# Performance work log

Measured on AMD Instinct MI355X. Metric: run time of the kernel, lower is better.

Reference implementation:

```python
import jax, jax.numpy as jnp
import numpy as np

B, N, M = 256, 2207, 16          # graphs per batch, nodes per graph, mid_channel
E = 16777216                      # total edges in the batched graph
C1, C2 = 12, 4                    # global_conv1_dim, global_conv2_dim
H1, H2 = 256, 64                  # FC hidden sizes
EPS = 1e-5                        # LayerNorm / BatchNorm eps
BN_SCALE = 1.0 / np.sqrt(1.0 + EPS)  # eval BatchNorm with running_mean=0, running_var=1


def setup_inputs() -> dict:
    ks = jax.random.split(jax.random.key(0), 16)
    def nrm(i, shape, s):
        return jax.random.normal(ks[i], shape, jnp.float32) * s
    return {
        "x": jax.random.normal(ks[0], (B * N, 1), jnp.float32),
        "edge_index": jax.random.randint(ks[1], (2, E), 0, B * N, dtype=jnp.int32),
        "edge_weight": jax.random.uniform(ks[2], (E,), jnp.float32),
        # GraphConv: lin_rel (with bias) on aggregated neighbors + lin_root on self
        "w_root": nrm(3, (1, M), 0.5),
        "w_rel": nrm(4, (1, M), 0.5),
        "b_rel": jnp.full((M,), 0.01, jnp.float32),
        # LayerNorm over (num_nodes, mid_channel)
        "ln_g": jnp.ones((N, M), jnp.float32),
        "ln_b": jnp.zeros((N, M), jnp.float32),
        # 1x1 conv stacks
        "gc1_w": nrm(5, (C1, M), 0.3), "gc1_b": nrm(6, (C1,), 0.1),
        "bn1_g": jnp.ones((C1,), jnp.float32), "bn1_b": jnp.zeros((C1,), jnp.float32),
        "gc2_w": nrm(7, (C2, C1), 0.3), "gc2_b": nrm(8, (C2,), 0.1),
        "bn2_g": jnp.ones((C2,), jnp.float32), "bn2_b": jnp.zeros((C2,), jnp.float32),
        # FC stack (weights stored [in, out])
        "fc_w1": nrm(9, (C2 * N, H1), 0.02), "fc_b1": jnp.full((H1,), 0.01, jnp.float32),
        "fbn1_g": jnp.ones((H1,), jnp.float32), "fbn1_b": jnp.zeros((H1,), jnp.float32),
        "fc_w2": nrm(10, (H1, H2), 0.1), "fc_b2": jnp.full((H2,), 0.01, jnp.float32),
        "fbn2_g": jnp.ones((H2,), jnp.float32), "fbn2_b": jnp.zeros((H2,), jnp.float32),
        "fc1_w": nrm(11, (H2, 1), 0.1), "fc1_b": jnp.full((1,), 0.01, jnp.float32),
    }


def reference(x, edge_index, edge_weight, w_root, w_rel, b_rel, ln_g, ln_b,
              gc1_w, gc1_b, bn1_g, bn1_b, gc2_w, gc2_b, bn2_g, bn2_b,
              fc_w1, fc_b1, fbn1_g, fbn1_b, fc_w2, fc_b2, fbn2_g, fbn2_b,
              fc1_w, fc1_b):
    src, dst = edge_index[0], edge_index[1]
    # GraphConv: gather source features, weight, scatter-add to destinations
    agg = jax.ops.segment_sum(x[src] * edge_weight[:, None], dst, num_segments=B * N)
    h = jax.nn.relu(agg @ w_rel + b_rel + x @ w_root)          # [B*N, M]
    h = h.reshape(B, N, M)
    # LayerNorm over (N, M) per sample (biased variance, as in torch)
    mu = h.mean(axis=(1, 2), keepdims=True)
    var = ((h - mu) ** 2).mean(axis=(1, 2), keepdims=True)
    h = (h - mu) * jax.lax.rsqrt(var + EPS) * ln_g + ln_b
    h = h.transpose(0, 2, 1)                                   # [B, M, N]
    # 1x1 conv -> relu -> eval-BN (rm=0, rv=1)
    y = jax.nn.relu(jnp.einsum('oc,bcn->bon', gc1_w, h) + gc1_b[None, :, None])
    y = y * (BN_SCALE * bn1_g)[None, :, None] + bn1_b[None, :, None]
    y = jax.nn.relu(jnp.einsum('oc,bcn->bon', gc2_w, y) + gc2_b[None, :, None])
    y = y * (BN_SCALE * bn2_g)[None, :, None] + bn2_b[None, :, None]
    z = y.reshape(B, C2 * N)                                   # channel-major flatten, matches torch view
    z = z @ fc_w1 + fc_b1
    z = jax.nn.relu(z * (BN_SCALE * fbn1_g) + fbn1_b)
    z = z @ fc_w2 + fc_b2
    z = jax.nn.relu(z * (BN_SCALE * fbn2_g) + fbn2_b)
    return z @ fc1_w + fc1_b                                   # [B, 1]
```

## Files before the change

### kernel.cpp

```cpp
#include <hip/hip_runtime.h>
#include <hip/hip_bf16.h>

#define BB   256
#define NN   2207
#define MM   16
#define EE   16777216
#define CC1  12
#define CC2  4
#define HH1  256
#define HH2  64
#define KK1  (CC2*NN)
#define LN_EPS 1e-5f
#define BN_SCALE 0.9999950000374997f
#define NBK  256
#define MAGIC 1946067ull
#define EPB  4096
#define TPB  512
#define EPT  (EPB/TPB)
#define NBLK (EE/EPB)

static __device__ __forceinline__ unsigned bucket_of(int d) {
    return (unsigned)(((unsigned long long)(unsigned)d * MAGIC) >> 32);
}

__global__ __launch_bounds__(TPB, 8)
void k_place2(const int* __restrict__ src, const int* __restrict__ dst,
              const float* __restrict__ ew, const float* __restrict__ x,
              uint2* __restrict__ recs, unsigned short* __restrict__ stab)
{
    __shared__ __align__(16) uint2 pl[EPB];
    __shared__ unsigned int hist[NBK], start[NBK];
    __shared__ unsigned int wtot[4];

    const int t = threadIdx.x;
    if (t < NBK) hist[t] = 0;
    __syncthreads();

    const int i4base = blockIdx.x * (EPB/4);
    unsigned pk[EPT];
    float    pv[EPT];
    #pragma unroll
    for (int q = 0; q < EPT/4; ++q) {
        int i4 = i4base + q*TPB + t;
        int4   s4 = reinterpret_cast<const int4*>(src)[i4];
        int4   d4 = reinterpret_cast<const int4*>(dst)[i4];
        float4 w4 = reinterpret_cast<const float4*>(ew)[i4];
        {
            unsigned b_ = bucket_of(d4.x);
            unsigned r_ = atomicAdd(&hist[b_], 1u);
            pk[q*4+0] = (b_ << 24) | (r_ << 12) | (unsigned)(d4.x - (int)(b_*NN));
            pv[q*4+0] = x[s4.x] * w4.x;
        }
        {
            unsigned b_ = bucket_of(d4.y);
            unsigned r_ = atomicAdd(&hist[b_], 1u);
            pk[q*4+1] = (b_ << 24) | (r_ << 12) | (unsigned)(d4.y - (int)(b_*NN));
            pv[q*4+1] = x[s4.y] * w4.y;
        }
        {
            unsigned b_ = bucket_of(d4.z);
            unsigned r_ = atomicAdd(&hist[b_], 1u);
            pk[q*4+2] = (b_ << 24) | (r_ << 12) | (unsigned)(d4.z - (int)(b_*NN));
            pv[q*4+2] = x[s4.z] * w4.z;
        }
        {
            unsigned b_ = bucket_of(d4.w);
            unsigned r_ = atomicAdd(&hist[b_], 1u);
            pk[q*4+3] = (b_ << 24) | (r_ << 12) | (unsigned)(d4.w - (int)(b_*NN));
            pv[q*4+3] = x[s4.w] * w4.w;
        }
    }
    __syncthreads();

    if (t < NBK) {
        unsigned h = hist[t], v = h;
        #pragma unroll
        for (int off = 1; off < 64; off <<= 1) {
            unsigned u = __shfl_up(v, off);
            if ((t & 63) >= off) v += u;
        }
        start[t] = v - h;
        if ((t & 63) == 63) wtot[t >> 6] = v;
    }
    __syncthreads();
    if (t < NBK) {
        const int w = t >> 6;
        unsigned wo = 0;
        if (w > 0) wo += wtot[0];
        if (w > 1) wo += wtot[1];
        if (w > 2) wo += wtot[2];
        start[t] += wo;
        stab[blockIdx.x * NBK + t] = (unsigned short)(start[t]);
    }
    __syncthreads();

    #pragma unroll
    for (int e = 0; e < EPT; ++e) {
        unsigned b_ = pk[e] >> 24;
        unsigned r_ = (pk[e] >> 12) & 0xFFFu;
        pl[start[b_] + r_] = make_uint2(pk[e] & 0xFFFu, __float_as_uint(pv[e]));
    }
    __syncthreads();

    uint4* dst4 = reinterpret_cast<uint4*>(recs + (size_t)blockIdx.x * EPB);
    const uint4* src4 = reinterpret_cast<const uint4*>(pl);
    #pragma unroll
    for (int q = 0; q < EPB/2/TPB; ++q)
        dst4[q*TPB + t] = src4[q*TPB + t];
}

#define RTPB 256
__global__ __launch_bounds__(RTPB, 8)
void k_replay2(const uint2* __restrict__ recs, const unsigned short* __restrict__ stab,
               float* __restrict__ paggr, int rspl)
{
    __shared__ float acc[NN];
    const int t = threadIdx.x;
    const int j = blockIdx.x & (NBK - 1);
    const int r = blockIdx.x >> 8;
    const int kpr = NBLK / rspl;
    for (int n = t; n < NN; n += RTPB) acc[n] = 0.f;
    __syncthreads();

    const int gid = t >> 4, l16 = t & 15;
    const int kb0 = r * kpr;
    for (int kb_i = gid; kb_i < kpr; kb_i += RTPB/16) {
        const int kb = kb0 + kb_i;
        unsigned s0 = stab[(size_t)kb * NBK + j];
        unsigned s1 = (j < NBK-1) ? (unsigned)stab[(size_t)kb * NBK + j + 1]
                                  : (unsigned)EPB;
        const uint2* rp = recs + (size_t)kb * EPB;
        for (unsigned u = s0 + (unsigned)l16; u < s1; u += 16u) {
            uint2 rec = rp[u];
            atomicAdd(&acc[rec.x], __uint_as_float(rec.y));
        }
    }
    __syncthreads();
    float* pa = paggr + ((size_t)r * NBK + j) * NN;
    for (int n = t; n < NN; n += RTPB) pa[n] = acc[n];
}

__global__ __launch_bounds__(512)
void k_ln_conv(const float* __restrict__ x, const float* __restrict__ paggr,
              const float* __restrict__ w_root, const float* __restrict__ w_rel,
              const float* __restrict__ b_rel,
              const float* __restrict__ ln_g, const float* __restrict__ ln_b,
              const float* __restrict__ gc1_w, const float* __restrict__ gc1_b,
              const float* __restrict__ bn1_g, const float* __restrict__ bn1_b,
              const float* __restrict__ gc2_w, const float* __restrict__ gc2_b,
              const float* __restrict__ bn2_g, const float* __restrict__ bn2_b,
              float* __restrict__ z, int rspl)
{
    __shared__ float xs[NN], acc[NN];
    __shared__ float gw1[CC1*MM], gb1[CC1], sb1[CC1], tb1[CC1];
    __shared__ float gw2[CC2*CC1], gb2[CC2], sb2[CC2], tb2[CC2];
    __shared__ float redS[8], redQ[8];
    __shared__ float s_mu, s_rs;

    const int b = blockIdx.x, t = threadIdx.x;
    const float* xb = x + b*NN;
    for (int n = t; n < NN; n += 512) {
        xs[n] = xb[n];
        float a = 0.f;
        for (int r = 0; r < rspl; ++r)
            a += paggr[((size_t)r * NBK + b) * NN + n];
        acc[n] = a;
    }
    if (t < CC1*MM) gw1[t] = gc1_w[t];
    if (t >= 192 && t < 192+CC1) { int o = t-192; gb1[o]=gc1_b[o]; sb1[o]=BN_SCALE*bn1_g[o]; tb1[o]=bn1_b[o]; }
    if (t >= 208 && t < 208+CC2*CC1) gw2[t-208] = gc2_w[t-208];
    if (t >= 240 && t < 240+CC2) { int p=t-240; gb2[p]=gc2_b[p]; sb2[p]=BN_SCALE*bn2_g[p]; tb2[p]=bn2_b[p]; }

    float wr[MM], br[MM], wo[MM];
    #pragma unroll
    for (int m = 0; m < MM; ++m) { wr[m]=w_rel[m]; br[m]=b_rel[m]; wo[m]=w_root[m]; }
    __syncthreads();

    float S = 0.f, Q = 0.f;
    for (int n = t; n < NN; n += 512) {
        float a = acc[n], xv = xs[n];
        #pragma unroll
        for (int m = 0; m < MM; ++m) {
            float h = fmaxf(fmaf(a, wr[m], fmaf(xv, wo[m], br[m])), 0.f);
            S += h; Q += h*h;
        }
    }
    #pragma unroll
    for (int off = 32; off; off >>= 1) { S += __shfl_down(S, off); Q += __shfl_down(Q, off); }
    if ((t & 63) == 0) { redS[t>>6] = S; redQ[t>>6] = Q; }
    __syncthreads();
    if (t == 0) {
        float SS = 0.f, QQ = 0.f;
        #pragma unroll
        for (int i = 0; i < 8; ++i) { SS += redS[i]; QQ += redQ[i]; }
        const float inv = 1.f / (float)(NN*MM);
        float mu = SS * inv;
        float var = QQ * inv - mu*mu;
        s_mu = mu; s_rs = rsqrtf(var + LN_EPS);
    }
    __syncthreads();
    const float mu = s_mu, rs = s_rs;

    float* zb = z + (size_t)b * KK1;
    for (int n = t; n < NN; n += 512) {
        float a = acc[n], xv = xs[n];
        float hn[MM];
        const float4* g4  = reinterpret_cast<const float4*>(ln_g + n*MM);
        const float4* be4 = reinterpret_cast<const float4*>(ln_b + n*MM);
        #pragma unroll
        for (int q = 0; q < 4; ++q) {
            float4 g = g4[q], be = be4[q];
            float gg[4]  = {g.x, g.y, g.z, g.w};
            float bb_[4] = {be.x, be.y, be.z, be.w};
            #pragma unroll
            for (int j = 0; j < 4; ++j) {
                int m = q*4 + j;
                float h = fmaxf(fmaf(a, wr[m], fmaf(xv, wo[m], br[m])), 0.f);
                hn[m] = (h - mu) * rs * gg[j] + bb_[j];
            }
        }
        float y1[CC1];
        #pragma unroll
        for (int o = 0; o < CC1; ++o) {
            float a1 = gb1[o];
            #pragma unroll
            for (int m = 0; m < MM; ++m) a1 = fmaf(gw1[o*MM+m], hn[m], a1);
            y1[o] = fmaxf(a1, 0.f) * sb1[o] + tb1[o];
        }
        #pragma unroll
        for (int p = 0; p < CC2; ++p) {
            float a2 = gb2[p];
            #pragma unroll
            for (int o = 0; o < CC1; ++o) a2 = fmaf(gw2[p*CC1+o], y1[o], a2);
            zb[p*NN + n] = fmaxf(a2, 0.f) * sb2[p] + tb2[p];
        }
    }
}

#define GK_CHUNK 288
__global__ __launch_bounds__(256)
void k_fc1_part(const float* __restrict__ z, const float* __restrict__ W1,
                float* __restrict__ out1_part)
{
    __shared__ float zs[64*36];
    __shared__ float ws_[32*68];
    const int bt = blockIdx.x, jt = blockIdx.y, ks = blockIdx.z;
    const int t = threadIdx.x;
    const int tb = t >> 4, tj = t & 15;
    const int k0 = ks * GK_CHUNK;
    const int kend = min(k0 + GK_CHUNK, KK1);
    float acc[4][4] = {};
    const int zrow = t >> 2, zcol = (t & 3) * 8;
    const int wrow = t >> 3, wcol = (t & 7) * 8;

    for (int kc = k0; kc < kend; kc += 32) {
        const float* zsrc = z + (size_t)(bt*64 + zrow)*KK1 + kc + zcol;
        #pragma unroll
        for (int q = 0; q < 2; ++q) {
            int k = kc + zcol + q*4;
            float4 v;
            if (k + 3 < kend) v = *reinterpret_cast<const float4*>(zsrc + q*4);
            else {
                v.x = (k+0 < kend) ? zsrc[q*4+0] : 0.f;
                v.y = (k+1 < kend) ? zsrc[q*4+1] : 0.f;
                v.z = (k+2 < kend) ? zsrc[q*4+2] : 0.f;
                v.w = (k+3 < kend) ? zsrc[q*4+3] : 0.f;
            }
            *reinterpret_cast<float4*>(&zs[zrow*36 + zcol + q*4]) = v;
        }
        {
            int k = kc + wrow;
            const float* wsrc = W1 + (size_t)k*HH1 + jt*64 + wcol;
            #pragma unroll
            for (int q = 0; q < 2; ++q) {
                float4 v;
                if (k < kend) v = *reinterpret_cast<const float4*>(wsrc + q*4);
                else v = float4{0.f,0.f,0.f,0.f};
                *reinterpret_cast<float4*>(&ws_[wrow*68 + wcol + q*4]) = v;
            }
        }
        __syncthreads();
        #pragma unroll
        for (int kk = 0; kk < 32; ++kk) {
            float4 w4 = *reinterpret_cast<const float4*>(&ws_[kk*68 + tj*4]);
            float zv[4], wv[4] = {w4.x, w4.y, w4.z, w4.w};
            #pragma unroll
            for (int ib = 0; ib < 4; ++ib) zv[ib] = zs[(tb*4+ib)*36 + kk];
            #pragma unroll
            for (int ib = 0; ib < 4; ++ib)
                #pragma unroll
                for (int ij = 0; ij < 4; ++ij)
                    acc[ib][ij] = fmaf(zv[ib], wv[ij], acc[ib][ij]);
        }
        __syncthreads();
    }
    #pragma unroll
    for (int ib = 0; ib < 4; ++ib) {
        int row = bt*64 + tb*4 + ib;
        float4 v = make_float4(acc[ib][0], acc[ib][1], acc[ib][2], acc[ib][3]);
        *reinterpret_cast<float4*>(
            &out1_part[((size_t)ks*256 + row)*HH1 + jt*64 + tj*4]) = v;
    }
}

__global__ __launch_bounds__(256)
void k_tail_part(const float* __restrict__ out1_part,
            const float* __restrict__ fc_b1, const float* __restrict__ fbn1_g,
            const float* __restrict__ fbn1_b,
            const float* __restrict__ W2, const float* __restrict__ fc_b2,
            const float* __restrict__ fbn2_g, const float* __restrict__ fbn2_b,
            const float* __restrict__ fc1_w, const float* __restrict__ fc1_b,
            float* __restrict__ out)
{
    __shared__ float o1s[HH1];
    const int b = blockIdx.x, t = threadIdx.x;
    float raw = fc_b1[t];
    #pragma unroll 4
    for (int ks = 0; ks < 31; ++ks)
        raw += out1_part[((size_t)ks*256 + b)*HH1 + t];
    o1s[t] = fmaxf(raw * (BN_SCALE * fbn1_g[t]) + fbn1_b[t], 0.f);
    __syncthreads();
    if (t < HH2) {
        float acc = fc_b2[t];
        #pragma unroll 4
        for (int j = 0; j < HH1; ++j) acc = fmaf(o1s[j], W2[j*HH2 + t], acc);
        float v2 = fmaxf(acc * (BN_SCALE * fbn2_g[t]) + fbn2_b[t], 0.f);
        float c = v2 * fc1_w[t];
        #pragma unroll
        for (int off = 32; off; off >>= 1) c += __shfl_down(c, off);
        if (t == 0) out[b] = c + fc1_b[0];
    }
}

__global__ __launch_bounds__(256)
void k_edge(const int* __restrict__ src, const int* __restrict__ dst,
            const float* __restrict__ ew, const float* __restrict__ x,
            float* __restrict__ agg)
{
    int i = blockIdx.x * 256 + threadIdx.x;
    const int4   s4 = reinterpret_cast<const int4*>(src)[i];
    const int4   d4 = reinterpret_cast<const int4*>(dst)[i];
    const float4 w4 = reinterpret_cast<const float4*>(ew)[i];
    unsafeAtomicAdd(&agg[d4.x], x[s4.x] * w4.x);
    unsafeAtomicAdd(&agg[d4.y], x[s4.y] * w4.y);
    unsafeAtomicAdd(&agg[d4.z], x[s4.z] * w4.z);
    unsafeAtomicAdd(&agg[d4.w], x[s4.w] * w4.w);
}

__global__ __launch_bounds__(256)
void k_sample(const float* __restrict__ x, const float* __restrict__ agg,
              const float* __restrict__ w_root, const float* __restrict__ w_rel,
              const float* __restrict__ b_rel,
              const float* __restrict__ ln_g, const float* __restrict__ ln_b,
              const float* __restrict__ gc1_w, const float* __restrict__ gc1_b,
              const float* __restrict__ bn1_g, const float* __restrict__ bn1_b,
              const float* __restrict__ gc2_w, const float* __restrict__ gc2_b,
              const float* __restrict__ bn2_g, const float* __restrict__ bn2_b,
              float* __restrict__ z)
{
    __shared__ float xs[NN], as[NN];
    __shared__ float gw1[CC1*MM], gb1[CC1], sb1[CC1], tb1[CC1];
    __shared__ float gw2[CC2*CC1], gb2[CC2], sb2[CC2], tb2[CC2];
    __shared__ float redS[4], redQ[4];
    __shared__ float s_mu, s_rs;

    const int b = blockIdx.x, t = threadIdx.x;
    const float* xb = x + b*NN;
    const float* ab = agg + b*NN;
    for (int n = t; n < NN; n += 256) { xs[n] = xb[n]; as[n] = ab[n]; }
    if (t < CC1*MM) gw1[t] = gc1_w[t];
    if (t >= 192 && t < 192+CC1) { int o = t-192; gb1[o]=gc1_b[o]; sb1[o]=BN_SCALE*bn1_g[o]; tb1[o]=bn1_b[o]; }
    if (t >= 208 && t < 208+CC2*CC1) gw2[t-208] = gc2_w[t-208];
    if (t >= 240 && t < 240+CC2) { int p=t-240; gb2[p]=gc2_b[p]; sb2[p]=BN_SCALE*bn2_g[p]; tb2[p]=bn2_b[p]; }

    float wr[MM], br[MM], wo[MM];
    #pragma unroll
    for (int m = 0; m < MM; ++m) { wr[m]=w_rel[m]; br[m]=b_rel[m]; wo[m]=w_root[m]; }
    __syncthreads();

    float S = 0.f, Q = 0.f;
    for (int n = t; n < NN; n += 256) {
        float a = as[n], xv = xs[n];
        #pragma unroll
        for (int m = 0; m < MM; ++m) {
            float h = fmaxf(fmaf(a, wr[m], fmaf(xv, wo[m], br[m])), 0.f);
            S += h; Q += h*h;
        }
    }
    #pragma unroll
    for (int off = 32; off; off >>= 1) { S += __shfl_down(S, off); Q += __shfl_down(Q, off); }
    if ((t & 63) == 0) { redS[t>>6] = S; redQ[t>>6] = Q; }
    __syncthreads();
    if (t == 0) {
        float SS = redS[0]+redS[1]+redS[2]+redS[3];
        float QQ = redQ[0]+redQ[1]+redQ[2]+redQ[3];
        const float inv = 1.f / (float)(NN*MM);
        float mu = SS * inv;
        float var = QQ * inv - mu*mu;
        s_mu = mu; s_rs = rsqrtf(var + LN_EPS);
    }
    __syncthreads();
    const float mu = s_mu, rs = s_rs;

    float* zb = z + (size_t)b * KK1;
    for (int n = t; n < NN; n += 256) {
        float a = as[n], xv = xs[n];
        float hn[MM];
        const float4* g4  = reinterpret_cast<const float4*>(ln_g + n*MM);
        const float4* be4 = reinterpret_cast<const float4*>(ln_b + n*MM);
        #pragma unroll
        for (int q = 0; q < 4; ++q) {
            float4 g = g4[q], be = be4[q];
            float gg[4]  = {g.x, g.y, g.z, g.w};
            float bb_[4] = {be.x, be.y, be.z, be.w};
            #pragma unroll
            for (int j = 0; j < 4; ++j) {
                int m = q*4 + j;
                float h = fmaxf(fmaf(a, wr[m], fmaf(xv, wo[m], br[m])), 0.f);
                hn[m] = (h - mu) * rs * gg[j] + bb_[j];
            }
        }
        float y1[CC1];
        #pragma unroll
        for (int o = 0; o < CC1; ++o) {
            float a1 = gb1[o];
            #pragma unroll
            for (int m = 0; m < MM; ++m) a1 = fmaf(gw1[o*MM+m], hn[m], a1);
            y1[o] = fmaxf(a1, 0.f) * sb1[o] + tb1[o];
        }
        #pragma unroll
        for (int p = 0; p < CC2; ++p) {
            float a2 = gb2[p];
            #pragma unroll
            for (int o = 0; o < CC1; ++o) a2 = fmaf(gw2[p*CC1+o], y1[o], a2);
            zb[p*NN + n] = fmaxf(a2, 0.f) * sb2[p] + tb2[p];
        }
    }
}

__global__ __launch_bounds__(256)
void k_fc1(const float* __restrict__ z, const float* __restrict__ W1,
           float* __restrict__ out1_raw)
{
    __shared__ float zs[64*36];
    __shared__ float ws_[32*68];
    const int bt = blockIdx.x, jt = blockIdx.y, ks = blockIdx.z;
    const int t = threadIdx.x;
    const int tb = t >> 4, tj = t & 15;
    const int k0 = ks * GK_CHUNK;
    const int kend = min(k0 + GK_CHUNK, KK1);
    float acc[4][4] = {};
    const int zrow = t >> 2, zcol = (t & 3) * 8;
    const int wrow = t >> 3, wcol = (t & 7) * 8;

    for (int kc = k0; kc < kend; kc += 32) {
        const float* zsrc = z + (size_t)(bt*64 + zrow)*KK1 + kc + zcol;
        #pragma unroll
        for (int q = 0; q < 2; ++q) {
            int k = kc + zcol + q*4;
            float4 v;
            if (k + 3 < kend) v = *reinterpret_cast<const float4*>(zsrc + q*4);
            else {
                v.x = (k+0 < kend) ? zsrc[q*4+0] : 0.f;
                v.y = (k+1 < kend) ? zsrc[q*4+1] : 0.f;
                v.z = (k+2 < kend) ? zsrc[q*4+2] : 0.f;
                v.w = (k+3 < kend) ? zsrc[q*4+3] : 0.f;
            }
            *reinterpret_cast<float4*>(&zs[zrow*36 + zcol + q*4]) = v;
        }
        {
            int k = kc + wrow;
            const float* wsrc = W1 + (size_t)k*HH1 + jt*64 + wcol;
            #pragma unroll
            for (int q = 0; q < 2; ++q) {
                float4 v;
                if (k < kend) v = *reinterpret_cast<const float4*>(wsrc + q*4);
                else v = float4{0.f,0.f,0.f,0.f};
                *reinterpret_cast<float4*>(&ws_[wrow*68 + wcol + q*4]) = v;
            }
        }
        __syncthreads();
        #pragma unroll
        for (int kk = 0; kk < 32; ++kk) {
            float4 w4 = *reinterpret_cast<const float4*>(&ws_[kk*68 + tj*4]);
            float zv[4], wv[4] = {w4.x, w4.y, w4.z, w4.w};
            #pragma unroll
            for (int ib = 0; ib < 4; ++ib) zv[ib] = zs[(tb*4+ib)*36 + kk];
            #pragma unroll
            for (int ib = 0; ib < 4; ++ib)
                #pragma unroll
                for (int ij = 0; ij < 4; ++ij)
                    acc[ib][ij] = fmaf(zv[ib], wv[ij], acc[ib][ij]);
        }
        __syncthreads();
    }
    #pragma unroll
    for (int ib = 0; ib < 4; ++ib) {
        int row = bt*64 + tb*4 + ib;
        #pragma unroll
        for (int ij = 0; ij < 4; ++ij)
            unsafeAtomicAdd(&out1_raw[row*HH1 + jt*64 + tj*4 + ij], acc[ib][ij]);
    }
}

__global__ __launch_bounds__(256)
void k_tail(const float* __restrict__ out1_raw,
            const float* __restrict__ fc_b1, const float* __restrict__ fbn1_g,
            const float* __restrict__ fbn1_b,
            const float* __restrict__ W2, const float* __restrict__ fc_b2,
            const float* __restrict__ fbn2_g, const float* __restrict__ fbn2_b,
            const float* __restrict__ fc1_w, const float* __restrict__ fc1_b,
            float* __restrict__ out)
{
    __shared__ float o1s[HH1];
    const int b = blockIdx.x, t = threadIdx.x;
    float raw = out1_raw[b*HH1 + t] + fc_b1[t];
    o1s[t] = fmaxf(raw * (BN_SCALE * fbn1_g[t]) + fbn1_b[t], 0.f);
    __syncthreads();
    if (t < HH2) {
        float acc = fc_b2[t];
        #pragma unroll 4
        for (int j = 0; j < HH1; ++j) acc = fmaf(o1s[j], W2[j*HH2 + t], acc);
        float v2 = fmaxf(acc * (BN_SCALE * fbn2_g[t]) + fbn2_b[t], 0.f);
        float c = v2 * fc1_w[t];
        #pragma unroll
        for (int off = 32; off; off >>= 1) c += __shfl_down(c, off);
        if (t == 0) out[b] = c + fc1_b[0];
    }
}

extern "C" void kernel_launch(void* const* d_in, const int* in_sizes, int n_in,
                              void* d_out, int out_size, void* d_ws, size_t ws_size,
                              hipStream_t stream)
{
    const float* x      = (const float*)d_in[0];
    const int*   ei     = (const int*)  d_in[1];
    const float* ew     = (const float*)d_in[2];
    const float* w_root = (const float*)d_in[3];
    const float* w_rel  = (const float*)d_in[4];
    const float* b_rel  = (const float*)d_in[5];
    const float* ln_g   = (const float*)d_in[6];
    const float* ln_b   = (const float*)d_in[7];
    const float* gc1_w  = (const float*)d_in[8];
    const float* gc1_b  = (const float*)d_in[9];
    const float* bn1_g  = (const float*)d_in[10];
    const float* bn1_b  = (const float*)d_in[11];
    const float* gc2_w  = (const float*)d_in[12];
    const float* gc2_b  = (const float*)d_in[13];
    const float* bn2_g  = (const float*)d_in[14];
    const float* bn2_b  = (const float*)d_in[15];
    const float* fc_w1  = (const float*)d_in[16];
    const float* fc_b1  = (const float*)d_in[17];
    const float* fbn1_g = (const float*)d_in[18];
    const float* fbn1_b = (const float*)d_in[19];
    const float* fc_w2  = (const float*)d_in[20];
    const float* fc_b2  = (const float*)d_in[21];
    const float* fbn2_g = (const float*)d_in[22];
    const float* fbn2_b = (const float*)d_in[23];
    const float* fc1_w  = (const float*)d_in[24];
    const float* fc1_b  = (const float*)d_in[25];
    float* out = (float*)d_out;

    char* ws = (char*)d_ws;
    const size_t off_recs  = 0;
    const size_t off_stab  = off_recs + (size_t)NBLK*EPB*8;
    const size_t off_paggr = off_stab + (size_t)NBLK*NBK*2;
    const size_t o1p_sz    = (size_t)31*HH1*256*4;

    int rspl = 8;
    size_t pg_sz   = (size_t)rspl*NBK*NN*4;
    if (pg_sz < o1p_sz) pg_sz = o1p_sz;
    size_t off_zbuf = off_paggr + pg_sz;
    size_t need     = off_zbuf + (size_t)BB*KK1*4;
    if (ws_size < need) {
        rspl = 4;
        pg_sz = (size_t)rspl*NBK*NN*4;
        off_zbuf = off_paggr + pg_sz;
        need = off_zbuf + (size_t)BB*KK1*4;
    }

    if (ws_size >= need) {
        uint2*          recs  = (uint2*)(ws + off_recs);
        unsigned short* stab  = (unsigned short*)(ws + off_stab);
        float*          paggr = (float*)(ws + off_paggr);
        float*          zbuf  = (float*)(ws + off_zbuf);
        float*          o1p   = (float*)(ws + off_paggr);

        k_place2<<<NBLK, TPB, 0, stream>>>(ei, ei + EE, ew, x, recs, stab);
        k_replay2<<<NBK*rspl, RTPB, 0, stream>>>(recs, stab, paggr, rspl);
        k_ln_conv<<<BB, 512, 0, stream>>>(x, paggr,
                                         w_root, w_rel, b_rel, ln_g, ln_b,
                                         gc1_w, gc1_b, bn1_g, bn1_b,
                                         gc2_w, gc2_b, bn2_g, bn2_b, zbuf, rspl);
        k_fc1_part<<<dim3(4,4,31), 256, 0, stream>>>(zbuf, fc_w1, o1p);
        k_tail_part<<<BB, 256, 0, stream>>>(o1p, fc_b1, fbn1_g, fbn1_b,
                                       fc_w2, fc_b2, fbn2_g, fbn2_b,
                                       fc1_w, fc1_b, out);
    } else {
        float* agg      = (float*)(ws);
        float* zbuf     = (float*)(ws + 2259968);
        float* out1_raw = (float*)(ws + 2259968 + 9039872);

        hipMemsetAsync(agg,      0, (size_t)BB*NN*sizeof(float),  stream);
        hipMemsetAsync(out1_raw, 0, (size_t)BB*HH1*sizeof(float), stream);

        k_edge<<<EE/4/256, 256, 0, stream>>>(ei, ei + EE, ew, x, agg);
        k_sample<<<BB, 256, 0, stream>>>(x, agg, w_root, w_rel, b_rel, ln_g, ln_b,
                                         gc1_w, gc1_b, bn1_g, bn1_b,
                                         gc2_w, gc2_b, bn2_g, bn2_b, zbuf);
        k_fc1<<<dim3(4,4,31), 256, 0, stream>>>(zbuf, fc_w1, out1_raw);
        k_tail<<<BB, 256, 0, stream>>>(out1_raw, fc_b1, fbn1_g, fbn1_b,
                                       fc_w2, fc_b2, fbn2_g, fbn2_b,
                                       fc1_w, fc1_b, out);
    }
}
```

Before: 346.3 us.

## Defer x gather to replay and scatter records directly to global memory

The placement kernel no longer gathers x[src]. It packs the source index into the record key (src<<12 | local dst) and stores the raw edge weight instead. The x gather and multiply move into the replay kernel. The shared-memory staging buffer and its coalesced copy-out are also removed, so each thread writes its records straight to their sorted positions in global memory. This trims shared memory and syncs in placement, at the cost of uncoalesced global stores and random x reads inside the replay atomic loop. Packing src into 20 bits relies on B*N being below 2^20.

```diff
diff --git a/kernel.cpp b/kernel.cpp
--- a/kernel.cpp
+++ b/kernel.cpp
@@ -24,11 +24,10 @@
 }
 
 __global__ __launch_bounds__(TPB, 8)
-void k_place2(const int* __restrict__ src, const int* __restrict__ dst,
-              const float* __restrict__ ew, const float* __restrict__ x,
+void k_place4(const int* __restrict__ src, const int* __restrict__ dst,
+              const float* __restrict__ ew,
               uint2* __restrict__ recs, unsigned short* __restrict__ stab)
 {
-    __shared__ __align__(16) uint2 pl[EPB];
     __shared__ unsigned int hist[NBK], start[NBK];
     __shared__ unsigned int wtot[4];
 
@@ -37,38 +36,31 @@
     __syncthreads();
 
     const int i4base = blockIdx.x * (EPB/4);
-    unsigned pk[EPT];
-    float    pv[EPT];
+    unsigned key[EPT];
+    float    wv[EPT];
+    unsigned short rk[EPT];
+    unsigned char  bk[EPT];
     #pragma unroll
     for (int q = 0; q < EPT/4; ++q) {
         int i4 = i4base + q*TPB + t;
         int4   s4 = reinterpret_cast<const int4*>(src)[i4];
         int4   d4 = reinterpret_cast<const int4*>(dst)[i4];
         float4 w4 = reinterpret_cast<const float4*>(ew)[i4];
-        {
-            unsigned b_ = bucket_of(d4.x);
-            unsigned r_ = atomicAdd(&hist[b_], 1u);
-            pk[q*4+0] = (b_ << 24) | (r_ << 12) | (unsigned)(d4.x - (int)(b_*NN));
-            pv[q*4+0] = x[s4.x] * w4.x;
-        }
-        {
-            unsigned b_ = bucket_of(d4.y);
-            unsigned r_ = atomicAdd(&hist[b_], 1u);
-            pk[q*4+1] = (b_ << 24) | (r_ << 12) | (unsigned)(d4.y - (int)(b_*NN));
-            pv[q*4+1] = x[s4.y] * w4.y;
-        }
-        {
-            unsigned b_ = bucket_of(d4.z);
-            unsigned r_ = atomicAdd(&hist[b_], 1u);
-            pk[q*4+2] = (b_ << 24) | (r_ << 12) | (unsigned)(d4.z - (int)(b_*NN));
-            pv[q*4+2] = x[s4.z] * w4.z;
-        }
-        {
-            unsigned b_ = bucket_of(d4.w);
-            unsigned r_ = atomicAdd(&hist[b_], 1u);
-            pk[q*4+3] = (b_ << 24) | (r_ << 12) | (unsigned)(d4.w - (int)(b_*NN));
-            pv[q*4+3] = x[s4.w] * w4.w;
-        }
+        unsigned b0 = bucket_of(d4.x), b1 = bucket_of(d4.y);
+        unsigned b2 = bucket_of(d4.z), b3 = bucket_of(d4.w);
+        unsigned r0 = atomicAdd(&hist[b0], 1u);
+        unsigned r1 = atomicAdd(&hist[b1], 1u);
+        unsigned r2 = atomicAdd(&hist[b2], 1u);
+        unsigned r3 = atomicAdd(&hist[b3], 1u);
+        key[q*4+0] = ((unsigned)s4.x << 12) | (unsigned)(d4.x - (int)(b0*NN));
+        key[q*4+1] = ((unsigned)s4.y << 12) | (unsigned)(d4.y - (int)(b1*NN));
+        key[q*4+2] = ((unsigned)s4.z << 12) | (unsigned)(d4.z - (int)(b2*NN));
+        key[q*4+3] = ((unsigned)s4.w << 12) | (unsigned)(d4.w - (int)(b3*NN));
+        wv[q*4+0] = w4.x; wv[q*4+1] = w4.y; wv[q*4+2] = w4.z; wv[q*4+3] = w4.w;
+        rk[q*4+0] = (unsigned short)r0; rk[q*4+1] = (unsigned short)r1;
+        rk[q*4+2] = (unsigned short)r2; rk[q*4+3] = (unsigned short)r3;
+        bk[q*4+0] = (unsigned char)b0; bk[q*4+1] = (unsigned char)b1;
+        bk[q*4+2] = (unsigned char)b2; bk[q*4+3] = (unsigned char)b3;
     }
     __syncthreads();
 
@@ -94,25 +86,17 @@
     }
     __syncthreads();
 
-    #pragma unroll
-    for (int e = 0; e < EPT; ++e) {
-        unsigned b_ = pk[e] >> 24;
-        unsigned r_ = (pk[e] >> 12) & 0xFFFu;
-        pl[start[b_] + r_] = make_uint2(pk[e] & 0xFFFu, __float_as_uint(pv[e]));
-    }
-    __syncthreads();
-
-    uint4* dst4 = reinterpret_cast<uint4*>(recs + (size_t)blockIdx.x * EPB);
-    const uint4* src4 = reinterpret_cast<const uint4*>(pl);
-    #pragma unroll
-    for (int q = 0; q < EPB/2/TPB; ++q)
-        dst4[q*TPB + t] = src4[q*TPB + t];
+    uint2* rb = recs + (size_t)blockIdx.x * EPB;
+    #pragma unroll
+    for (int e = 0; e < EPT; ++e)
+        rb[start[bk[e]] + (unsigned)rk[e]] =
+            make_uint2(key[e], __float_as_uint(wv[e]));
 }
 
 #define RTPB 256
 __global__ __launch_bounds__(RTPB, 8)
-void k_replay2(const uint2* __restrict__ recs, const unsigned short* __restrict__ stab,
-               float* __restrict__ paggr, int rspl)
+void k_replay3(const uint2* __restrict__ recs, const unsigned short* __restrict__ stab,
+               const float* __restrict__ x, float* __restrict__ paggr, int rspl)
 {
     __shared__ float acc[NN];
     const int t = threadIdx.x;
@@ -132,7 +116,8 @@
         const uint2* rp = recs + (size_t)kb * EPB;
         for (unsigned u = s0 + (unsigned)l16; u < s1; u += 16u) {
             uint2 rec = rp[u];
-            atomicAdd(&acc[rec.x], __uint_as_float(rec.y));
+            atomicAdd(&acc[rec.x & 0xFFFu],
+                      x[rec.x >> 12] * __uint_as_float(rec.y));
         }
     }
     __syncthreads();
@@ -586,8 +571,8 @@
         float*          zbuf  = (float*)(ws + off_zbuf);
         float*          o1p   = (float*)(ws + off_paggr);
 
-        k_place2<<<NBLK, TPB, 0, stream>>>(ei, ei + EE, ew, x, recs, stab);
-        k_replay2<<<NBK*rspl, RTPB, 0, stream>>>(recs, stab, paggr, rspl);
+        k_place4<<<NBLK, TPB, 0, stream>>>(ei, ei + EE, ew, recs, stab);
+        k_replay3<<<NBK*rspl, RTPB, 0, stream>>>(recs, stab, x, paggr, rspl);
         k_ln_conv<<<BB, 512, 0, stream>>>(x, paggr,
                                          w_root, w_rel, b_rel, ln_g, ln_b,
                                          gc1_w, gc1_b, bn1_g, bn1_b,
```

Measured after the change: 314.5 us. 9.2% less time.
